# Optimization experiments

Measured on AMD Instinct MI355X. Metric: run time of the kernel, lower is better.

## Reference

```python
import jax, jax.numpy as jnp
import numpy as np

B, N, ENC, DEC, ATT = 32, 4096, 1024, 512, 512


def setup_inputs() -> dict:
    key = jax.random.key(0)
    ks = jax.random.split(key, 8)
    s_enc = 1.0 / np.sqrt(ENC)
    s_dec = 1.0 / np.sqrt(DEC)
    s_att = 1.0 / np.sqrt(ATT)
    return {
        "encoder_out": jax.random.normal(ks[0], (B, N, ENC), jnp.float32),
        "decoder_hidden": jax.random.normal(ks[1], (B, DEC), jnp.float32),
        "W_enc": jax.random.uniform(ks[2], (ENC, ATT), jnp.float32, -s_enc, s_enc),
        "b_enc": jax.random.uniform(ks[3], (ATT,), jnp.float32, -s_enc, s_enc),
        "W_dec": jax.random.uniform(ks[4], (DEC, ATT), jnp.float32, -s_dec, s_dec),
        "b_dec": jax.random.uniform(ks[5], (ATT,), jnp.float32, -s_dec, s_dec),
        "w_full": jax.random.uniform(ks[6], (ATT,), jnp.float32, -s_att, s_att),
        "b_full": jax.random.uniform(ks[7], (), jnp.float32, -s_att, s_att),
    }


def reference(encoder_out, decoder_hidden, W_enc, b_enc, W_dec, b_dec, w_full, b_full):
    # att1: [B, N, ATT]; att2: [B, 1, ATT]
    att1 = jnp.einsum('bne,ea->bna', encoder_out, W_enc) + b_enc
    att2 = (decoder_hidden @ W_dec + b_dec)[:, None, :]
    att = jax.nn.relu(att1 + att2)
    e = jnp.einsum('bna,a->bn', att, w_full) + b_full  # [B, N]
    alpha = jax.nn.softmax(e, axis=1)
    awe = jnp.einsum('bne,bn->be', encoder_out, alpha)  # weighted encoding [B, ENC]
    return awe, alpha
```

## Files before the change

### kernel.cpp

```cpp
#include <hip/hip_runtime.h>

#define B_ 32
#define N_ 4096
#define ENC_ 1024
#define DEC_ 512
#define ATT_ 512

typedef __attribute__((ext_vector_type(8))) short short8;
typedef __attribute__((ext_vector_type(4))) float f32x4;

__device__ __forceinline__ short f2bf(float f) {
  union { float f; unsigned u; } x; x.f = f;
  unsigned r = (x.u + 0x7FFFu + ((x.u >> 16) & 1u)) >> 16;
  return (short)r;
}

__device__ __forceinline__ void gl_lds16(const float* g, void* l) {
  __builtin_amdgcn_global_load_lds(
      (const __attribute__((address_space(1))) unsigned int*)g,
      (__attribute__((address_space(3))) unsigned int*)l, 16, 0, 0);
}

extern "C" __global__ void __launch_bounds__(256) prep_kernel(
    const float* __restrict__ dh, const float* __restrict__ W_dec,
    const float* __restrict__ b_dec, const float* __restrict__ b_enc,
    const float* __restrict__ W_enc,
    float* __restrict__ att2, short* __restrict__ Wfrag)
{
  if (blockIdx.x < B_) {
    __shared__ float dhs[DEC_];
    int b = blockIdx.x;
    for (int i = threadIdx.x; i < DEC_; i += 256) dhs[i] = dh[b * DEC_ + i];
    __syncthreads();
    for (int a = threadIdx.x; a < ATT_; a += 256) {
      float s = b_dec[a] + b_enc[a];
      for (int k = 0; k < DEC_; ++k) s += dhs[k] * W_dec[k * ATT_ + a];
      att2[b * ATT_ + a] = s;
    }
  } else {
    int idx = (blockIdx.x - B_) * 256 + threadIdx.x;
    int l = idx & 63;
    int g = (idx >> 6) & 31;
    int c = idx >> 11;
    int col = c * 16 + (l & 15);
    int kb = g * 32 + (l >> 4) * 8;
    short8 p;
#pragma unroll
    for (int j = 0; j < 8; ++j) p[j] = f2bf(W_enc[(kb + j) * ATT_ + col]);
    *(short8*)(Wfrag + ((long)idx << 3)) = p;
  }
}

extern "C" __global__ void __launch_bounds__(256, 3) gemm_e_kernel(
    const float* __restrict__ enc, const short* __restrict__ Wfrag,
    const float* __restrict__ att2, const float* __restrict__ w_full,
    float* __restrict__ e_part)
{
  __shared__ __align__(16) float As[2][64 * 64];
  __shared__ float e_red[64][4];

  const int tid = threadIdx.x;
  const int lane = tid & 63;
  const int w = tid >> 6;
  const int blk = blockIdx.x;
  const int g16 = blk >> 4;
  const int h = (blk >> 3) & 1;
  const int p = g16 * 8 + (blk & 7);
  const int b = p >> 6;
  const int n0 = (p & 63) * 64;

  const int qv = lane >> 4;
  const int ch = lane & 15;

  const float* asrc[4];
#pragma unroll
  for (int j = 0; j < 4; ++j) {
    int rl = j * 4 + qv;
    asrc[j] = enc + (long)(b * N_ + n0 + w * 16 + rl) * ENC_ +
              ((ch ^ ((qv + (j & 1) * 4) & 7)) << 2);
  }

  const int abase0 = ch * 256 + (((qv * 2 + 0) ^ (ch & 7)) << 4);
  const int abase1 = ch * 256 + (((qv * 2 + 1) ^ (ch & 7)) << 4);

  const short* bptr = Wfrag + (long)(h * 16 + w * 4) * 16384 + lane * 8;

  f32x4 acc[4][4] = {};

  {
    char* d = (char*)(&As[0][0]) + (w << 12);
#pragma unroll
    for (int j = 0; j < 4; ++j) gl_lds16(asrc[j], d + j * 1024);
  }
  __syncthreads();

#pragma unroll
  for (int t = 0; t < 16; ++t) {
    const int cur = t & 1;
    if (t + 1 < 16) {
      char* d = (char*)(&As[cur ^ 1][0]) + (w << 12);
#pragma unroll
      for (int j = 0; j < 4; ++j)
        gl_lds16(asrc[j] + (t + 1) * 64, d + j * 1024);
    }
#pragma unroll
    for (int ks = 0; ks < 2; ++ks) {
      short8 bfg[4];
#pragma unroll
      for (int cc = 0; cc < 4; ++cc)
        bfg[cc] = *(const short8*)(bptr + cc * 16384 + (2 * t + ks) * 512);
      short8 af[4];
#pragma unroll
      for (int r = 0; r < 4; ++r) {
        f32x4 lo = *(const f32x4*)((const char*)(&As[cur][0]) +
                                   (abase0 + r * 4096 + ks * 128));
        f32x4 hi = *(const f32x4*)((const char*)(&As[cur][0]) +
                                   (abase1 + r * 4096 + ks * 128));
#pragma unroll
        for (int j = 0; j < 4; ++j) {
          af[r][j] = f2bf(lo[j]);
          af[r][j + 4] = f2bf(hi[j]);
        }
      }
      __builtin_amdgcn_s_setprio(1);
#pragma unroll
      for (int cc = 0; cc < 4; ++cc)
#pragma unroll
        for (int r = 0; r < 4; ++r)
          acc[r][cc] = __builtin_amdgcn_mfma_f32_16x16x32_bf16(
              af[r], bfg[cc], acc[r][cc], 0, 0, 0);
      __builtin_amdgcn_s_setprio(0);
    }
    __syncthreads();
  }

  const int lq = lane >> 4, lr = lane & 15;
  float at2v[4], wv[4];
#pragma unroll
  for (int c = 0; c < 4; ++c) {
    int col = h * 256 + w * 64 + c * 16 + lr;
    at2v[c] = att2[b * ATT_ + col];
    wv[c] = w_full[col];
  }
#pragma unroll
  for (int r = 0; r < 4; ++r) {
#pragma unroll
    for (int j = 0; j < 4; ++j) {
      float s = 0.f;
#pragma unroll
      for (int c = 0; c < 4; ++c)
        s += fmaxf(acc[r][c][j] + at2v[c], 0.f) * wv[c];
      s += __shfl_xor(s, 1); s += __shfl_xor(s, 2);
      s += __shfl_xor(s, 4); s += __shfl_xor(s, 8);
      if (lr == 0) e_red[r * 16 + lq * 4 + j][w] = s;
    }
  }
  __syncthreads();
  if (tid < 64) {
    float ev = e_red[tid][0] + e_red[tid][1] + e_red[tid][2] + e_red[tid][3];
    e_part[(long)h * (B_ * N_) + b * N_ + n0 + tid] = ev;
  }
}

extern "C" __global__ void __launch_bounds__(256) softmax_kernel(
    const float* __restrict__ e, float* __restrict__ alpha)
{
  int b = blockIdx.x, tid = threadIdx.x;
  float v[16];
  float m = -1e30f;
#pragma unroll
  for (int i = 0; i < 16; ++i) {
    int idx = b * N_ + i * 256 + tid;
    v[i] = e[idx] + e[B_ * N_ + idx];
    m = fmaxf(m, v[i]);
  }
  for (int off = 1; off < 64; off <<= 1) m = fmaxf(m, __shfl_xor(m, off));
  __shared__ float redm[4];
  if ((tid & 63) == 0) redm[tid >> 6] = m;
  __syncthreads();
  m = fmaxf(fmaxf(redm[0], redm[1]), fmaxf(redm[2], redm[3]));
  float s = 0.f;
#pragma unroll
  for (int i = 0; i < 16; ++i) { v[i] = expf(v[i] - m); s += v[i]; }
  for (int off = 1; off < 64; off <<= 1) s += __shfl_xor(s, off);
  __shared__ float reds[4];
  if ((tid & 63) == 0) reds[tid >> 6] = s;
  __syncthreads();
  s = reds[0] + reds[1] + reds[2] + reds[3];
  float inv = 1.0f / s;
#pragma unroll
  for (int i = 0; i < 16; ++i) alpha[b * N_ + i * 256 + tid] = v[i] * inv;
}

extern "C" __global__ void __launch_bounds__(256) awe_part_kernel(
    const float* __restrict__ enc, const float* __restrict__ alpha,
    float* __restrict__ part)
{
  __shared__ float als[256];
  __shared__ f32x4 red[256];
  int bi = blockIdx.x;
  int b = bi & 31, cchunk = (bi >> 5) & 3, nchunk = bi >> 7;
  int t = threadIdx.x;
  int n0 = nchunk * 256;
  als[t] = alpha[b * N_ + n0 + t];
  __syncthreads();
  int tcol = t & 63, tn = t >> 6;
  const float* base = enc + (long)b * N_ * ENC_ + (long)n0 * ENC_ +
                      cchunk * 256 + tcol * 4;
  f32x4 acc = {};
  for (int i = tn; i < 256; i += 4) {
    f32x4 vv = *(const f32x4*)(base + (long)i * ENC_);
    acc += als[i] * vv;
  }
  red[t] = acc;
  __syncthreads();
  if (t < 64) {
    f32x4 s = red[t] + red[t + 64] + red[t + 128] + red[t + 192];
    *(f32x4*)(&part[(long)nchunk * 32768 + b * 1024 + cchunk * 256 + t * 4]) = s;
  }
}

extern "C" __global__ void __launch_bounds__(256) awe_reduce_kernel(
    const float* __restrict__ part, float* __restrict__ awe)
{
  int i = blockIdx.x * 256 + threadIdx.x;
  float s = 0.f;
#pragma unroll
  for (int p = 0; p < 16; ++p) s += part[(long)p * 32768 + i];
  awe[i] = s;
}

extern "C" void kernel_launch(void* const* d_in, const int* in_sizes, int n_in,
                              void* d_out, int out_size, void* d_ws, size_t ws_size,
                              hipStream_t stream) {
  const float* enc    = (const float*)d_in[0];
  const float* dh     = (const float*)d_in[1];
  const float* W_enc  = (const float*)d_in[2];
  const float* b_enc  = (const float*)d_in[3];
  const float* W_dec  = (const float*)d_in[4];
  const float* b_dec  = (const float*)d_in[5];
  const float* w_full = (const float*)d_in[6];
  float* out = (float*)d_out;

  char* ws = (char*)d_ws;
  float* att2  = (float*)ws;
  short* Wfrag = (short*)(ws + 65536);
  float* e_buf = (float*)(ws + 65536 + 1048576);
  float* part  = (float*)(ws + 65536 + 1048576 + 1048576);

  hipLaunchKernelGGL(prep_kernel, dim3(B_ + 256), dim3(256), 0, stream,
                     dh, W_dec, b_dec, b_enc, W_enc, att2, Wfrag);
  hipLaunchKernelGGL(gemm_e_kernel, dim3(4096), dim3(256), 0, stream,
                     enc, Wfrag, att2, w_full, e_buf);
  hipLaunchKernelGGL(softmax_kernel, dim3(B_), dim3(256), 0, stream,
                     e_buf, out + B_ * ENC_);
  hipLaunchKernelGGL(awe_part_kernel, dim3(2048), dim3(256), 0, stream,
                     enc, out + B_ * ENC_, part);
  hipLaunchKernelGGL(awe_reduce_kernel, dim3(128), dim3(256), 0, stream,
                     part, out);
}
```

Before: 356.2 us.

## Double-buffer B fragments in registers and use packed bf16 conversion instruction

The GEMM inner loop now prefetches the next k-step's W_enc fragments from global memory into a second register set while MFMAs consume the current set, hiding global load latency behind compute. The scalar per-element f32-to-bf16 rounding code is replaced by the hardware v_cvt_pk_bf16_f32 instruction, which converts two floats per instruction and cuts VALU work. The cost is more live VGPRs from the extra fragment buffers, which could pressure occupancy under launch_bounds(256,3). The rounding behaviour of the hardware conversion may also differ slightly on NaN handling.

```diff
diff --git a/kernel.cpp b/kernel.cpp
--- a/kernel.cpp
+++ b/kernel.cpp
@@ -8,11 +8,18 @@
 
 typedef __attribute__((ext_vector_type(8))) short short8;
 typedef __attribute__((ext_vector_type(4))) float f32x4;
+typedef __attribute__((ext_vector_type(4))) unsigned u32x4;
 
 __device__ __forceinline__ short f2bf(float f) {
   union { float f; unsigned u; } x; x.f = f;
   unsigned r = (x.u + 0x7FFFu + ((x.u >> 16) & 1u)) >> 16;
   return (short)r;
+}
+
+__device__ __forceinline__ unsigned cvtpk(float a, float b) {
+  unsigned r;
+  asm("v_cvt_pk_bf16_f32 %0, %1, %2" : "=v"(r) : "v"(a), "v"(b));
+  return r;
 }
 
 __device__ __forceinline__ void gl_lds16(const float* g, void* l) {
@@ -86,12 +93,16 @@
   const short* bptr = Wfrag + (long)(h * 16 + w * 4) * 16384 + lane * 8;
 
   f32x4 acc[4][4] = {};
+  short8 bfgA[4], bfgB[4];
 
   {
     char* d = (char*)(&As[0][0]) + (w << 12);
 #pragma unroll
     for (int j = 0; j < 4; ++j) gl_lds16(asrc[j], d + j * 1024);
   }
+#pragma unroll
+  for (int cc = 0; cc < 4; ++cc)
+    bfgA[cc] = *(const short8*)(bptr + cc * 16384);
   __syncthreads();
 
 #pragma unroll
@@ -103,24 +114,23 @@
       for (int j = 0; j < 4; ++j)
         gl_lds16(asrc[j] + (t + 1) * 64, d + j * 1024);
     }
-#pragma unroll
-    for (int ks = 0; ks < 2; ++ks) {
-      short8 bfg[4];
+    {
 #pragma unroll
       for (int cc = 0; cc < 4; ++cc)
-        bfg[cc] = *(const short8*)(bptr + cc * 16384 + (2 * t + ks) * 512);
+        bfgB[cc] = *(const short8*)(bptr + cc * 16384 + (2 * t + 1) * 512);
       short8 af[4];
 #pragma unroll
       for (int r = 0; r < 4; ++r) {
         f32x4 lo = *(const f32x4*)((const char*)(&As[cur][0]) +
-                                   (abase0 + r * 4096 + ks * 128));
+                                   (abase0 + r * 4096));
         f32x4 hi = *(const f32x4*)((const char*)(&As[cur][0]) +
-                                   (abase1 + r * 4096 + ks * 128));
-#pragma unroll
-        for (int j = 0; j < 4; ++j) {
-          af[r][j] = f2bf(lo[j]);
-          af[r][j + 4] = f2bf(hi[j]);
-        }
+                                   (abase1 + r * 4096));
+        union { u32x4 u; short8 s; } cv;
+        cv.u[0] = cvtpk(lo[0], lo[1]);
+        cv.u[1] = cvtpk(lo[2], lo[3]);
+        cv.u[2] = cvtpk(hi[0], hi[1]);
+        cv.u[3] = cvtpk(hi[2], hi[3]);
+        af[r] = cv.s;
       }
       __builtin_amdgcn_s_setprio(1);
 #pragma unroll
@@ -128,7 +138,36 @@
 #pragma unroll
         for (int r = 0; r < 4; ++r)
           acc[r][cc] = __builtin_amdgcn_mfma_f32_16x16x32_bf16(
-              af[r], bfg[cc], acc[r][cc], 0, 0, 0);
+              af[r], bfgA[cc], acc[r][cc], 0, 0, 0);
+      __builtin_amdgcn_s_setprio(0);
+    }
+    {
+      if (2 * t + 2 < 32) {
+#pragma unroll
+        for (int cc = 0; cc < 4; ++cc)
+          bfgA[cc] = *(const short8*)(bptr + cc * 16384 + (2 * t + 2) * 512);
+      }
+      short8 af[4];
+#pragma unroll
+      for (int r = 0; r < 4; ++r) {
+        f32x4 lo = *(const f32x4*)((const char*)(&As[cur][0]) +
+                                   (abase0 + r * 4096 + 128));
+        f32x4 hi = *(const f32x4*)((const char*)(&As[cur][0]) +
+                                   (abase1 + r * 4096 + 128));
+        union { u32x4 u; short8 s; } cv;
+        cv.u[0] = cvtpk(lo[0], lo[1]);
+        cv.u[1] = cvtpk(lo[2], lo[3]);
+        cv.u[2] = cvtpk(hi[0], hi[1]);
+        cv.u[3] = cvtpk(hi[2], hi[3]);
+        af[r] = cv.s;
+      }
+      __builtin_amdgcn_s_setprio(1);
+#pragma unroll
+      for (int cc = 0; cc < 4; ++cc)
+#pragma unroll
+        for (int r = 0; r < 4; ++r)
+          acc[r][cc] = __builtin_amdgcn_mfma_f32_16x16x32_bf16(
+              af[r], bfgB[cc], acc[r][cc], 0, 0, 0);
       __builtin_amdgcn_s_setprio(0);
     }
     __syncthreads();
```

Measured after the change: 326.0 us. 1.09x faster.
